# Performance work log

Measured on AMD Instinct MI355X. Metric: run time of the kernel, lower is better.

The kernel has to match this reference:

```python
import jax, jax.numpy as jnp
import numpy as np
import math

B, T, C, H = 8, 1024, 1024, 16
D = C // H  # head dim = 64
EPS = 1e-5


def layernorm(x, g, b):
    mu = jnp.mean(x, axis=-1, keepdims=True)
    var = jnp.var(x, axis=-1, keepdims=True)
    return (x - mu) * jax.lax.rsqrt(var + EPS) * g + b


def setup_inputs() -> dict:
    key = jax.random.key(0)
    ks = jax.random.split(key, 8)
    s = lambda fan_in: 1.0 / math.sqrt(fan_in)
    return {
        "x": jax.random.normal(ks[0], (B, T, C), jnp.float32),
        "Wqkv": jax.random.normal(ks[1], (C, 3 * C), jnp.float32) * s(C),
        "bqkv": jnp.zeros((3 * C,), jnp.float32),
        "Wproj": jax.random.normal(ks[2], (C, C), jnp.float32) * s(C),
        "bproj": jnp.zeros((C,), jnp.float32),
        "ln1_g": jnp.ones((C,), jnp.float32),
        "ln1_b": jnp.zeros((C,), jnp.float32),
        "ln2_g": jnp.ones((C,), jnp.float32),
        "ln2_b": jnp.zeros((C,), jnp.float32),
        "W1": jax.random.normal(ks[3], (C, 4 * C), jnp.float32) * s(C),
        "b1": jnp.zeros((4 * C,), jnp.float32),
        "W2": jax.random.normal(ks[4], (4 * C, C), jnp.float32) * s(4 * C),
        "b2": jnp.zeros((C,), jnp.float32),
    }


def reference(x, Wqkv, bqkv, Wproj, bproj, ln1_g, ln1_b, ln2_g, ln2_b, W1, b1, W2, b2):
    # --- self-attention on ln1(x) ---
    h = layernorm(x, ln1_g, ln1_b)
    qkv = h @ Wqkv + bqkv                          # [B,T,3C]
    q, k, v = jnp.split(qkv, 3, axis=-1)
    # [B,T,C] -> [B,H,T,D]
    q = q.reshape(B, T, H, D).transpose(0, 2, 1, 3)
    k = k.reshape(B, T, H, D).transpose(0, 2, 1, 3)
    v = v.reshape(B, T, H, D).transpose(0, 2, 1, 3)
    # NOTE: original uses 1/sqrt(3*n_embd//n_head), not 1/sqrt(head_dim)
    scale = 1.0 / math.sqrt(3 * C // H)
    attn = jnp.einsum("bhqd,bhkd->bhqk", q, k) * scale  # [B,H,T,T]
    causal = jnp.tril(jnp.ones((T, T), bool))
    attn = jnp.where(causal, attn, -jnp.inf)
    attn = jax.nn.softmax(attn, axis=-1)
    y = jnp.einsum("bhqk,bhkd->bhqd", attn, v)          # [B,H,T,D]
    y = y.transpose(0, 2, 1, 3).reshape(B, T, C)
    x = x + (y @ Wproj + bproj)
    # --- MLP on ln2(x) ---
    h2 = layernorm(x, ln2_g, ln2_b)
    x = x + (jax.nn.relu(h2 @ W1 + b1) @ W2 + b2)
    return x
```

## Files before the change

kernel.cpp:

```cpp
#include <hip/hip_runtime.h>

typedef __bf16 bf16;
typedef __bf16 bf16x8 __attribute__((ext_vector_type(8)));
typedef float f32x4 __attribute__((ext_vector_type(4)));

#define MFMA16(a, b, c) __builtin_amdgcn_mfma_f32_16x16x32_bf16(a, b, c, 0, 0, 0)

static constexpr int Bn = 8;
static constexpr int Tn = 1024;
static constexpr int Cn = 1024;
static constexpr int Hn = 16;

typedef const __attribute__((address_space(1))) unsigned int* gp_t;
typedef __attribute__((address_space(3))) unsigned int* lp_t;
__device__ __forceinline__ void gload_lds16(const bf16* g, bf16* l) {
    __builtin_amdgcn_global_load_lds((gp_t)(const void*)g, (lp_t)(void*)l, 16, 0, 0);
}

__global__ __launch_bounds__(256) void tcast_all(const float* __restrict__ Wqkv,
                                                 const float* __restrict__ Wproj,
                                                 const float* __restrict__ W1,
                                                 const float* __restrict__ W2,
                                                 bf16* __restrict__ WqkvT,
                                                 bf16* __restrict__ WprojT,
                                                 bf16* __restrict__ W1T,
                                                 bf16* __restrict__ W2T) {
    int bid = blockIdx.x;
    const float* in;
    bf16* out;
    int K, N;
    if (bid < 3072) {
        in = Wqkv; out = WqkvT; K = 1024; N = 3072;
    } else if (bid < 4096) {
        bid -= 3072; in = Wproj; out = WprojT; K = 1024; N = 1024;
    } else if (bid < 8192) {
        bid -= 4096; in = W1; out = W1T; K = 1024; N = 4096;
    } else {
        bid -= 8192; in = W2; out = W2T; K = 4096; N = 1024;
    }
    const int ntx = N / 32;
    const int n0 = (bid % ntx) * 32, k0 = (bid / ntx) * 32;
    __shared__ float tile[32][33];
    const int tx = threadIdx.x & 31, ty = threadIdx.x >> 5;
#pragma unroll
    for (int i = 0; i < 4; i++)
        tile[ty + 8 * i][tx] = in[(size_t)(k0 + ty + 8 * i) * N + n0 + tx];
    __syncthreads();
#pragma unroll
    for (int i = 0; i < 4; i++)
        out[(size_t)(n0 + ty + 8 * i) * K + k0 + tx] = (bf16)tile[tx][ty + 8 * i];
}

template <typename T>
__global__ __launch_bounds__(256) void ln_row(const T* __restrict__ x,
                                              const float* __restrict__ g,
                                              const float* __restrict__ be,
                                              bf16* __restrict__ out) {
    const int row = blockIdx.x, t = threadIdx.x;
    const T* xr = x + (size_t)row * Cn;
    float v[4], s = 0.f, s2 = 0.f;
#pragma unroll
    for (int i = 0; i < 4; i++) {
        v[i] = (float)xr[t + i * 256];
        s += v[i];
        s2 += v[i] * v[i];
    }
#pragma unroll
    for (int off = 32; off > 0; off >>= 1) {
        s += __shfl_down(s, off);
        s2 += __shfl_down(s2, off);
    }
    __shared__ float red[8];
    const int wave = t >> 6, lane = t & 63;
    if (lane == 0) {
        red[wave] = s;
        red[4 + wave] = s2;
    }
    __syncthreads();
    s = red[0] + red[1] + red[2] + red[3];
    s2 = red[4] + red[5] + red[6] + red[7];
    const float mu = s * (1.f / Cn);
    const float rstd = rsqrtf(s2 * (1.f / Cn) - mu * mu + 1e-5f);
    bf16* orow = out + (size_t)row * Cn;
#pragma unroll
    for (int i = 0; i < 4; i++) {
        int c = t + i * 256;
        orow[c] = (bf16)((v[i] - mu) * rstd * g[c] + be[c]);
    }
}

__global__ __launch_bounds__(256) void vtrans(const bf16* __restrict__ qkv,
                                              bf16* __restrict__ Vt) {
    __shared__ bf16 tile[64 * 72];
    const int tid = threadIdx.x;
    const int bh = blockIdx.x, b = bh >> 4, h = bh & 15;
    const int t0 = blockIdx.y * 64;
    const int r = tid >> 3, c = (tid & 7) * 8;
#pragma unroll
    for (int i = 0; i < 2; i++) {
        const int rr = r + i * 32;
        *(bf16x8*)(tile + rr * 72 + c) =
            *(const bf16x8*)(qkv + ((size_t)(b * Tn + t0 + rr)) * 3072 + 2 * Cn + h * 64 + c);
    }
    __syncthreads();
#pragma unroll
    for (int i = 0; i < 2; i++) {
        const int d = r + i * 32;
        bf16x8 v;
#pragma unroll
        for (int j = 0; j < 8; j++) v[j] = tile[(c + j) * 72 + d];
        *(bf16x8*)(Vt + ((size_t)bh * 64 + d) * Tn + t0 + c) = v;
    }
}

template <int TM, int TN, int BK, bool RELU, bool RESID, bool OUTBF16, typename RT>
__global__ __launch_bounds__(256, 2) void gemm_bt(const bf16* __restrict__ A,
                                                  const bf16* __restrict__ Bt,
                                                  const float* __restrict__ bias,
                                                  const RT* __restrict__ resid,
                                                  void* __restrict__ outp,
                                                  int M, int N, int K) {
    constexpr int MI = TM / 32;
    constexpr int NI = TN / 32;
    constexpr int CPR = BK / 8;
    constexpr int RPG = 64 / CPR;
    constexpr int AJ = TM / (4 * RPG);
    constexpr int BJ = TN / (4 * RPG);
    __shared__ __align__(16) bf16 As[TM * BK];
    __shared__ __align__(16) bf16 Bs[TN * BK];
    const int t = threadIdx.x;
    const int lane = t & 63, wave = t >> 6;
    const int lane15 = lane & 15, quad = lane >> 4;
    const int m0 = blockIdx.x * TM, n0 = blockIdx.y * TN;
    const int mb = (wave >> 1) * (TM / 2), nb = (wave & 1) * (TN / 2);

    const f32x4 zero4 = {0.f, 0.f, 0.f, 0.f};
    f32x4 acc[MI][NI];
#pragma unroll
    for (int i = 0; i < MI; i++)
#pragma unroll
        for (int j = 0; j < NI; j++) acc[i][j] = zero4;

    const int grow = lane / CPR;
    const int gsub = lane % CPR;

    for (int kt = 0; kt < K; kt += BK) {
#pragma unroll
        for (int j = 0; j < AJ; j++) {
            const int rj = wave * (AJ * RPG) + j * RPG + grow;
            const int cj = (gsub ^ (rj & 7)) * 8;
            gload_lds16(A + (size_t)(m0 + rj) * K + kt + cj,
                        As + (wave * (AJ * RPG) + j * RPG) * BK);
        }
#pragma unroll
        for (int j = 0; j < BJ; j++) {
            const int rj = wave * (BJ * RPG) + j * RPG + grow;
            const int cj = (gsub ^ (rj & 7)) * 8;
            gload_lds16(Bt + (size_t)(n0 + rj) * K + kt + cj,
                        Bs + (wave * (BJ * RPG) + j * RPG) * BK);
        }
        __syncthreads();
#pragma unroll
        for (int kk = 0; kk < BK / 32; kk++) {
            bf16x8 fa[MI], fb[NI];
#pragma unroll
            for (int mi = 0; mi < MI; mi++) {
                const int r = mb + mi * 16 + lane15;
                fa[mi] = *(const bf16x8*)(As + r * BK + (((kk * 4 + quad) ^ (r & 7)) * 8));
            }
#pragma unroll
            for (int ni = 0; ni < NI; ni++) {
                const int r = nb + ni * 16 + lane15;
                fb[ni] = *(const bf16x8*)(Bs + r * BK + (((kk * 4 + quad) ^ (r & 7)) * 8));
            }
#pragma unroll
            for (int mi = 0; mi < MI; mi++)
#pragma unroll
                for (int ni = 0; ni < NI; ni++)
                    acc[mi][ni] = MFMA16(fa[mi], fb[ni], acc[mi][ni]);
        }
        __syncthreads();
    }

    float bsv[NI];
#pragma unroll
    for (int ni = 0; ni < NI; ni++) bsv[ni] = bias[n0 + nb + ni * 16 + lane15];
#pragma unroll
    for (int mi = 0; mi < MI; mi++) {
#pragma unroll
        for (int reg = 0; reg < 4; reg++) {
            const int row = m0 + mb + mi * 16 + quad * 4 + reg;
#pragma unroll
            for (int ni = 0; ni < NI; ni++) {
                const int col = n0 + nb + ni * 16 + lane15;
                float v = acc[mi][ni][reg] + bsv[ni];
                if (RELU) v = v > 0.f ? v : 0.f;
                if (RESID) v += (float)resid[(size_t)row * N + col];
                if (OUTBF16)
                    ((bf16*)outp)[(size_t)row * N + col] = (bf16)v;
                else
                    ((float*)outp)[(size_t)row * N + col] = v;
            }
        }
    }
}

__global__ __launch_bounds__(256) void attn(const bf16* __restrict__ qkv,
                                            const bf16* __restrict__ Vt,
                                            bf16* __restrict__ y) {
    __shared__ __align__(16) bf16 Ks[2][64 * 64];
    __shared__ __align__(16) bf16 Vs[2][64 * 64];
    __shared__ __align__(16) bf16 Ones[16 * 64];
    __shared__ __align__(16) bf16 Ps[4][32 * 64];
    const int tid = threadIdx.x, lane = tid & 63, wave = tid >> 6;
    const int lane15 = lane & 15, quad = lane >> 4;
    const int b = blockIdx.x >> 4, h = blockIdx.x & 15;
    const int q0 = blockIdx.y * 128;
    const int qr0 = q0 + wave * 32;
    const float c1 = 0.10412043f;

    for (int i = tid; i < 16 * 64; i += 256) Ones[i] = (bf16)((i < 64) ? 1.0f : 0.0f);

    const int grow = lane >> 3;
    const int gcol = ((lane & 7) ^ grow) * 8;
    const int srow = wave * 16 + grow;
    const bf16* gK = qkv + ((size_t)(b * Tn + srow)) * 3072 + Cn + h * 64 + gcol;
    const bf16* gV = Vt + ((size_t)(blockIdx.x * 64 + srow)) * Tn + gcol;

    auto stage = [&](int kb, int p) {
        const int k0 = kb * 64;
#pragma unroll
        for (int j = 0; j < 2; j++) {
            gload_lds16(gK + (size_t)(k0 + j * 8) * 3072, &Ks[p][(wave * 16 + j * 8) * 64]);
            gload_lds16(gV + (size_t)(j * 8) * Tn + k0, &Vs[p][(wave * 16 + j * 8) * 64]);
        }
    };

    bf16x8 fq[2][2];
#pragma unroll
    for (int mi = 0; mi < 2; mi++) {
        const size_t qb = ((size_t)(b * Tn + qr0 + mi * 16 + lane15)) * 3072 + h * 64;
#pragma unroll
        for (int kk = 0; kk < 2; kk++)
            fq[mi][kk] = *(const bf16x8*)(qkv + qb + kk * 32 + quad * 8);
    }

    const f32x4 zero4 = {0.f, 0.f, 0.f, 0.f};
    f32x4 o[2][4], lacc[2];
#pragma unroll
    for (int mi = 0; mi < 2; mi++) {
        lacc[mi] = zero4;
#pragma unroll
        for (int ni = 0; ni < 4; ni++) o[mi][ni] = zero4;
    }

    stage(0, 0);
    const int nkb = q0 / 64 + 2;
    for (int kb = 0; kb < nkb; kb++) {
        const int p = kb & 1;
        const int k0 = kb * 64;
        __syncthreads();
        if (kb + 1 < nkb) stage(kb + 1, 1 - p);

        if (k0 <= qr0 + 31) {
            bf16x8 fk[4][2];
#pragma unroll
            for (int ni = 0; ni < 4; ni++) {
                const int r = ni * 16 + lane15;
#pragma unroll
                for (int kk = 0; kk < 2; kk++)
                    fk[ni][kk] = *(const bf16x8*)(&Ks[p][r * 64 + (((kk * 4 + quad) ^ (r & 7)) * 8)]);
            }
            f32x4 s[2][4];
#pragma unroll
            for (int mi = 0; mi < 2; mi++)
#pragma unroll
                for (int ni = 0; ni < 4; ni++) {
                    if (k0 + ni * 16 <= qr0 + mi * 16 + 15) {
                        f32x4 a = zero4;
                        a = MFMA16(fq[mi][0], fk[ni][0], a);
                        a = MFMA16(fq[mi][1], fk[ni][1], a);
                        s[mi][ni] = a;
                    }
                }
            const bool domask = (k0 + 63 > qr0);
#pragma unroll
            for (int mi = 0; mi < 2; mi++)
#pragma unroll
                for (int ni = 0; ni < 4; ni++) {
#pragma unroll
                    for (int r = 0; r < 4; r++) {
                        const int prow = mi * 16 + quad * 4 + r;
                        const int r7 = (quad * 4 + r) & 7;
                        const int paddr = prow * 64 + (((ni * 2 + (lane15 >> 3)) ^ r7) * 8) +
                                          (lane15 & 7);
                        float val;
                        if (domask && (k0 + ni * 16 > qr0 + mi * 16 + 15)) {
                            val = 0.f;
                        } else if (domask && (k0 + ni * 16 + 15 > qr0 + mi * 16)) {
                            const int key = k0 + ni * 16 + lane15;
                            const int row = qr0 + prow;
                            float L = (key > row) ? -1e30f : s[mi][ni][r] * c1;
                            val = __builtin_amdgcn_exp2f(L);
                        } else {
                            val = __builtin_amdgcn_exp2f(s[mi][ni][r] * c1);
                        }
                        Ps[wave][paddr] = (bf16)val;
                    }
                }
            bf16x8 fp[2][2];
#pragma unroll
            for (int mi = 0; mi < 2; mi++) {
                const int r = mi * 16 + lane15;
#pragma unroll
                for (int kk = 0; kk < 2; kk++)
                    fp[mi][kk] = *(const bf16x8*)(&Ps[wave][r * 64 + (((kk * 4 + quad) ^ (r & 7)) * 8)]);
            }
            const bool use_kk1 = (k0 + 32 <= qr0 + 31);
#pragma unroll
            for (int ni = 0; ni < 5; ni++) {
                bf16x8 fv0, fv1;
                if (ni < 4) {
                    const int r = ni * 16 + lane15;
                    fv0 = *(const bf16x8*)(&Vs[p][r * 64 + ((quad ^ (r & 7)) * 8)]);
                    fv1 = *(const bf16x8*)(&Vs[p][r * 64 + (((4 + quad) ^ (r & 7)) * 8)]);
                } else {
                    fv0 = *(const bf16x8*)(Ones + lane15 * 64 + quad * 8);
                    fv1 = *(const bf16x8*)(Ones + lane15 * 64 + 32 + quad * 8);
                }
#pragma unroll
                for (int mi = 0; mi < 2; mi++) {
                    f32x4* dst = (ni < 4) ? &o[mi][ni] : &lacc[mi];
                    f32x4 a = *dst;
                    a = MFMA16(fp[mi][0], fv0, a);
                    if (use_kk1) a = MFMA16(fp[mi][1], fv1, a);
                    *dst = a;
                }
            }
        }
    }

#pragma unroll
    for (int mi = 0; mi < 2; mi++)
#pragma unroll
        for (int r = 0; r < 4; r++) {
            float l = __shfl(lacc[mi][r], lane & 48);
            const float inv = 1.f / l;
            const size_t base = ((size_t)(b * Tn + qr0 + mi * 16 + quad * 4 + r)) * Cn + h * 64;
#pragma unroll
            for (int ni = 0; ni < 4; ni++)
                y[base + ni * 16 + lane15] = (bf16)(o[mi][ni][r] * inv);
        }
}

extern "C" void kernel_launch(void* const* d_in, const int* in_sizes, int n_in,
                              void* d_out, int out_size, void* d_ws, size_t ws_size,
                              hipStream_t stream) {
    const float* x = (const float*)d_in[0];
    const float* Wqkv = (const float*)d_in[1];
    const float* bqkv = (const float*)d_in[2];
    const float* Wproj = (const float*)d_in[3];
    const float* bproj = (const float*)d_in[4];
    const float* ln1g = (const float*)d_in[5];
    const float* ln1b = (const float*)d_in[6];
    const float* ln2g = (const float*)d_in[7];
    const float* ln2b = (const float*)d_in[8];
    const float* W1 = (const float*)d_in[9];
    const float* b1 = (const float*)d_in[10];
    const float* W2 = (const float*)d_in[11];
    const float* b2 = (const float*)d_in[12];
    float* out = (float*)d_out;

    char* ws = (char*)d_ws;
    size_t off = 0;
    auto alloc = [&](size_t bytes) {
        void* p = ws + off;
        off += (bytes + 255) & ~(size_t)255;
        return p;
    };
    bf16* WqkvT = (bf16*)alloc((size_t)3072 * 1024 * 2);
    bf16* WprojT = (bf16*)alloc((size_t)1024 * 1024 * 2);
    bf16* W1T = (bf16*)alloc((size_t)4096 * 1024 * 2);
    bf16* W2T = (bf16*)alloc((size_t)1024 * 4096 * 2);
    bf16* hbuf = (bf16*)alloc((size_t)8192 * 1024 * 2);
    bf16* qkvb = (bf16*)alloc((size_t)8192 * 3072 * 2);
    bf16* ybuf = (bf16*)alloc((size_t)8192 * 1024 * 2);
    bf16* vtb = (bf16*)alloc((size_t)8192 * 1024 * 2);
    bf16* x1b = (bf16*)alloc((size_t)8192 * 1024 * 2);
    bf16* a1 = qkvb;

    tcast_all<<<12288, 256, 0, stream>>>(Wqkv, Wproj, W1, W2, WqkvT, WprojT, W1T, W2T);

    ln_row<float><<<8192, 256, 0, stream>>>(x, ln1g, ln1b, hbuf);
    gemm_bt<128, 256, 64, false, false, true, float><<<dim3(64, 12), 256, 0, stream>>>(
        hbuf, WqkvT, bqkv, (const float*)nullptr, qkvb, 8192, 3072, 1024);
    vtrans<<<dim3(Bn * Hn, Tn / 64), 256, 0, stream>>>(qkvb, vtb);
    attn<<<dim3(Bn * Hn, Tn / 128), 256, 0, stream>>>(qkvb, vtb, ybuf);
    gemm_bt<128, 128, 128, false, true, true, float><<<dim3(64, 8), 256, 0, stream>>>(
        ybuf, WprojT, bproj, x, x1b, 8192, 1024, 1024);
    ln_row<bf16><<<8192, 256, 0, stream>>>(x1b, ln2g, ln2b, hbuf);
    gemm_bt<128, 256, 64, true, false, true, float><<<dim3(64, 16), 256, 0, stream>>>(
        hbuf, W1T, b1, (const float*)nullptr, a1, 8192, 4096, 1024);
    gemm_bt<128, 128, 128, false, true, false, bf16><<<dim3(64, 8), 256, 0, stream>>>(
        a1, W2T, b2, x1b, out, 8192, 1024, 4096);
}
```

Measured before the change: 440.4 us.

## Restructure attention into single-wave blocks reading K/V directly from global memory

```diff
diff --git a/kernel.cpp b/kernel.cpp
--- a/kernel.cpp
+++ b/kernel.cpp
@@ -205,36 +205,16 @@
     }
 }
 
-__global__ __launch_bounds__(256) void attn(const bf16* __restrict__ qkv,
-                                            const bf16* __restrict__ Vt,
-                                            bf16* __restrict__ y) {
-    __shared__ __align__(16) bf16 Ks[2][64 * 64];
-    __shared__ __align__(16) bf16 Vs[2][64 * 64];
-    __shared__ __align__(16) bf16 Ones[16 * 64];
-    __shared__ __align__(16) bf16 Ps[4][32 * 64];
-    const int tid = threadIdx.x, lane = tid & 63, wave = tid >> 6;
+__global__ __launch_bounds__(64, 3) void attn(const bf16* __restrict__ qkv,
+                                              const bf16* __restrict__ Vt,
+                                              bf16* __restrict__ y) {
+    __shared__ __align__(16) bf16 Ps[32 * 64];
+    const int lane = threadIdx.x & 63;
     const int lane15 = lane & 15, quad = lane >> 4;
-    const int b = blockIdx.x >> 4, h = blockIdx.x & 15;
-    const int q0 = blockIdx.y * 128;
-    const int qr0 = q0 + wave * 32;
+    const int bh = blockIdx.x, b = bh >> 4, h = bh & 15;
+    const int tile = 31 - (int)blockIdx.y;
+    const int qr0 = tile * 32;
     const float c1 = 0.10412043f;
-
-    for (int i = tid; i < 16 * 64; i += 256) Ones[i] = (bf16)((i < 64) ? 1.0f : 0.0f);
-
-    const int grow = lane >> 3;
-    const int gcol = ((lane & 7) ^ grow) * 8;
-    const int srow = wave * 16 + grow;
-    const bf16* gK = qkv + ((size_t)(b * Tn + srow)) * 3072 + Cn + h * 64 + gcol;
-    const bf16* gV = Vt + ((size_t)(blockIdx.x * 64 + srow)) * Tn + gcol;
-
-    auto stage = [&](int kb, int p) {
-        const int k0 = kb * 64;
-#pragma unroll
-        for (int j = 0; j < 2; j++) {
-            gload_lds16(gK + (size_t)(k0 + j * 8) * 3072, &Ks[p][(wave * 16 + j * 8) * 64]);
-            gload_lds16(gV + (size_t)(j * 8) * Tn + k0, &Vs[p][(wave * 16 + j * 8) * 64]);
-        }
-    };
 
     bf16x8 fq[2][2];
 #pragma unroll
@@ -245,6 +225,10 @@
             fq[mi][kk] = *(const bf16x8*)(qkv + qb + kk * 32 + quad * 8);
     }
 
+    bf16x8 fvone;
+#pragma unroll
+    for (int j = 0; j < 8; j++) fvone[j] = (bf16)(lane15 == 0 ? 1.0f : 0.0f);
+
     const f32x4 zero4 = {0.f, 0.f, 0.f, 0.f};
     f32x4 o[2][4], lacc[2];
 #pragma unroll
@@ -254,88 +238,83 @@
         for (int ni = 0; ni < 4; ni++) o[mi][ni] = zero4;
     }
 
-    stage(0, 0);
-    const int nkb = q0 / 64 + 2;
+    const int nkb = tile / 2 + 1;
     for (int kb = 0; kb < nkb; kb++) {
-        const int p = kb & 1;
         const int k0 = kb * 64;
-        __syncthreads();
-        if (kb + 1 < nkb) stage(kb + 1, 1 - p);
-
-        if (k0 <= qr0 + 31) {
-            bf16x8 fk[4][2];
+        bf16x8 fk[4][2];
+#pragma unroll
+        for (int ni = 0; ni < 4; ni++) {
+            if (k0 + ni * 16 <= qr0 + 31) {
+                const size_t ka = ((size_t)(b * Tn + k0 + ni * 16 + lane15)) * 3072 + Cn + h * 64;
+#pragma unroll
+                for (int kk = 0; kk < 2; kk++)
+                    fk[ni][kk] = *(const bf16x8*)(qkv + ka + kk * 32 + quad * 8);
+            }
+        }
+        f32x4 s[2][4];
+#pragma unroll
+        for (int mi = 0; mi < 2; mi++)
 #pragma unroll
             for (int ni = 0; ni < 4; ni++) {
-                const int r = ni * 16 + lane15;
-#pragma unroll
-                for (int kk = 0; kk < 2; kk++)
-                    fk[ni][kk] = *(const bf16x8*)(&Ks[p][r * 64 + (((kk * 4 + quad) ^ (r & 7)) * 8)]);
-            }
-            f32x4 s[2][4];
-#pragma unroll
-            for (int mi = 0; mi < 2; mi++)
-#pragma unroll
-                for (int ni = 0; ni < 4; ni++) {
-                    if (k0 + ni * 16 <= qr0 + mi * 16 + 15) {
-                        f32x4 a = zero4;
-                        a = MFMA16(fq[mi][0], fk[ni][0], a);
-                        a = MFMA16(fq[mi][1], fk[ni][1], a);
-                        s[mi][ni] = a;
+                if (k0 + ni * 16 <= qr0 + mi * 16 + 15) {
+                    f32x4 a = zero4;
+                    a = MFMA16(fq[mi][0], fk[ni][0], a);
+                    a = MFMA16(fq[mi][1], fk[ni][1], a);
+                    s[mi][ni] = a;
+                }
+            }
+        const bool domask = (k0 + 63 > qr0);
+#pragma unroll
+        for (int mi = 0; mi < 2; mi++)
+#pragma unroll
+            for (int ni = 0; ni < 4; ni++) {
+#pragma unroll
+                for (int r = 0; r < 4; r++) {
+                    const int prow = mi * 16 + quad * 4 + r;
+                    const int r7 = (quad * 4 + r) & 7;
+                    const int paddr =
+                        prow * 64 + (((ni * 2 + (lane15 >> 3)) ^ r7) * 8) + (lane15 & 7);
+                    float val;
+                    if (domask && (k0 + ni * 16 > qr0 + mi * 16 + 15)) {
+                        val = 0.f;
+                    } else if (domask && (k0 + ni * 16 + 15 > qr0 + mi * 16)) {
+                        const int key = k0 + ni * 16 + lane15;
+                        const int row = qr0 + prow;
+                        float L = (key > row) ? -1e30f : s[mi][ni][r] * c1;
+                        val = __builtin_amdgcn_exp2f(L);
+                    } else {
+                        val = __builtin_amdgcn_exp2f(s[mi][ni][r] * c1);
                     }
+                    Ps[paddr] = (bf16)val;
                 }
-            const bool domask = (k0 + 63 > qr0);
-#pragma unroll
-            for (int mi = 0; mi < 2; mi++)
-#pragma unroll
-                for (int ni = 0; ni < 4; ni++) {
-#pragma unroll
-                    for (int r = 0; r < 4; r++) {
-                        const int prow = mi * 16 + quad * 4 + r;
-                        const int r7 = (quad * 4 + r) & 7;
-                        const int paddr = prow * 64 + (((ni * 2 + (lane15 >> 3)) ^ r7) * 8) +
-                                          (lane15 & 7);
-                        float val;
-                        if (domask && (k0 + ni * 16 > qr0 + mi * 16 + 15)) {
-                            val = 0.f;
-                        } else if (domask && (k0 + ni * 16 + 15 > qr0 + mi * 16)) {
-                            const int key = k0 + ni * 16 + lane15;
-                            const int row = qr0 + prow;
-                            float L = (key > row) ? -1e30f : s[mi][ni][r] * c1;
-                            val = __builtin_amdgcn_exp2f(L);
-                        } else {
-                            val = __builtin_amdgcn_exp2f(s[mi][ni][r] * c1);
-                        }
-                        Ps[wave][paddr] = (bf16)val;
-                    }
-                }
-            bf16x8 fp[2][2];
+            }
+        bf16x8 fp[2][2];
+#pragma unroll
+        for (int mi = 0; mi < 2; mi++) {
+            const int r = mi * 16 + lane15;
+#pragma unroll
+            for (int kk = 0; kk < 2; kk++)
+                fp[mi][kk] = *(const bf16x8*)(&Ps[r * 64 + (((kk * 4 + quad) ^ (r & 7)) * 8)]);
+        }
+        const bool use_kk1 = (k0 + 32 <= qr0 + 31);
+#pragma unroll
+        for (int ni = 0; ni < 5; ni++) {
+            bf16x8 fv0, fv1;
+            if (ni < 4) {
+                const size_t va = ((size_t)(bh * 64 + ni * 16 + lane15)) * Tn + k0;
+                fv0 = *(const bf16x8*)(Vt + va + quad * 8);
+                fv1 = *(const bf16x8*)(Vt + va + 32 + quad * 8);
+            } else {
+                fv0 = fvone;
+                fv1 = fvone;
+            }
 #pragma unroll
             for (int mi = 0; mi < 2; mi++) {
-                const int r = mi * 16 + lane15;
-#pragma unroll
-                for (int kk = 0; kk < 2; kk++)
-                    fp[mi][kk] = *(const bf16x8*)(&Ps[wave][r * 64 + (((kk * 4 + quad) ^ (r & 7)) * 8)]);
-            }
-            const bool use_kk1 = (k0 + 32 <= qr0 + 31);
-#pragma unroll
-            for (int ni = 0; ni < 5; ni++) {
-                bf16x8 fv0, fv1;
-                if (ni < 4) {
-                    const int r = ni * 16 + lane15;
-                    fv0 = *(const bf16x8*)(&Vs[p][r * 64 + ((quad ^ (r & 7)) * 8)]);
-                    fv1 = *(const bf16x8*)(&Vs[p][r * 64 + (((4 + quad) ^ (r & 7)) * 8)]);
-                } else {
-                    fv0 = *(const bf16x8*)(Ones + lane15 * 64 + quad * 8);
-                    fv1 = *(const bf16x8*)(Ones + lane15 * 64 + 32 + quad * 8);
-                }
-#pragma unroll
-                for (int mi = 0; mi < 2; mi++) {
-                    f32x4* dst = (ni < 4) ? &o[mi][ni] : &lacc[mi];
-                    f32x4 a = *dst;
-                    a = MFMA16(fp[mi][0], fv0, a);
-                    if (use_kk1) a = MFMA16(fp[mi][1], fv1, a);
-                    *dst = a;
-                }
+                f32x4* dst = (ni < 4) ? &o[mi][ni] : &lacc[mi];
+                f32x4 a = *dst;
+                a = MFMA16(fp[mi][0], fv0, a);
+                if (use_kk1) a = MFMA16(fp[mi][1], fv1, a);
+                *dst = a;
             }
         }
     }
@@ -395,7 +374,7 @@
     gemm_bt<128, 256, 64, false, false, true, float><<<dim3(64, 12), 256, 0, stream>>>(
         hbuf, WqkvT, bqkv, (const float*)nullptr, qkvb, 8192, 3072, 1024);
     vtrans<<<dim3(Bn * Hn, Tn / 64), 256, 0, stream>>>(qkvb, vtb);
-    attn<<<dim3(Bn * Hn, Tn / 128), 256, 0, stream>>>(qkvb, vtb, ybuf);
+    attn<<<dim3(Bn * Hn, 32), 64, 0, stream>>>(qkvb, vtb, ybuf);
     gemm_bt<128, 128, 128, false, true, true, float><<<dim3(64, 8), 256, 0, stream>>>(
         ybuf, WprojT, bproj, x, x1b, 8192, 1024, 1024);
     ln_row<bf16><<<8192, 256, 0, stream>>>(x1b, ln2g, ln2b, hbuf);
```

After: 560.7 us. 1.27x slower.
